# Optimization experiments

Measured on AMD Instinct MI355X. Metric: run time of the kernel, lower is better.

## Reference

```python
import jax, jax.numpy as jnp
import numpy as np

K = 3
TAU = 1.0
EPS = 1e-8


def _route_dense(z, k, tau):
    """RouterTopK forward -> dense combine weights [N, L].
    Matches torch: topk values, softmax(topv/tau). Softmax is permutation
    invariant so sorted top_k gives identical math to sorted=False."""
    topi = jax.lax.top_k(z, k)[1]                      # [N, k] int32
    topv = jnp.take_along_axis(z, topi, axis=1)        # [N, k]
    w = jax.nn.softmax(topv / (tau + EPS), axis=1)     # [N, k]
    N, L = z.shape
    dw = jnp.zeros((N, L), z.dtype)
    dw = dw.at[jnp.arange(N)[:, None], topi].add(w)
    return dw


def _apply_mixture(x, dw, W):
    """y[n] = sum_e dw[n,e] * (W[e] @ x[n]).  Loop over the small fixed
    expert count (12); equivalent math to the sort+grouped-GEMM dispatch."""
    y = jnp.zeros((x.shape[0], W.shape[1]), x.dtype)
    for e in range(W.shape[0]):
        y = y + (x @ W[e].T) * dw[:, e:e + 1]
    return y


def setup_inputs() -> dict:
    key = jax.random.key(0)
    ks = jax.random.split(key, 8)
    B, T, D_in, H, D_out, L, d_addr = 4, 2048, 1024, 4096, 1024, 12, 64

    def unitize(U):
        U = U - U.mean(axis=1, keepdims=True)
        return U / (jnp.linalg.norm(U, axis=1, keepdims=True) + EPS)

    x = jax.random.normal(ks[0], (B, T, D_in), jnp.float32)
    P_w = jax.random.normal(ks[1], (d_addr, D_in), jnp.float32) / np.sqrt(D_in)
    U1 = unitize(jax.random.normal(ks[2], (L, d_addr), jnp.float32))
    U2 = unitize(jax.random.normal(ks[3], (L, d_addr), jnp.float32))
    U3 = unitize(jax.random.normal(ks[4], (L, d_addr), jnp.float32))
    W1 = jax.random.normal(ks[5], (L, H, D_in), jnp.float32)
    W1 = W1 / jnp.linalg.norm(W1.reshape(L, -1), axis=1)[:, None, None]
    W2 = jax.random.normal(ks[6], (L, D_out, H), jnp.float32)
    W2 = W2 / jnp.linalg.norm(W2.reshape(L, -1), axis=1)[:, None, None]
    b2 = jax.random.normal(ks[7], (L, D_out), jnp.float32)
    b2 = b2 / jnp.linalg.norm(b2, axis=1, keepdims=True)
    return {"x": x, "P_w": P_w, "U1": U1, "U2": U2, "U3": U3,
            "W1": W1, "W2": W2, "b2": b2}


def reference(x, P_w, U1, U2, U3, W1, W2, b2):
    B, T, D = x.shape
    x_flat = x.reshape(B * T, D)                       # [N, D_in]
    x_addr = x_flat @ P_w.T                            # [N, d_addr]
    dw1 = _route_dense(x_addr @ U1.T, K, TAU)          # [N, L]
    dw2 = _route_dense(x_addr @ U2.T, K, TAU)
    dw3 = _route_dense(x_addr @ U3.T, K, TAU)
    h = _apply_mixture(x_flat, dw1, W1)                # [N, H]
    h = jax.nn.gelu(h, approximate=False)              # nn.GELU (exact)
    y = _apply_mixture(h, dw2, W2)                     # [N, D_out]
    y = y + dw3 @ b2                                   # grouped bias add
    return y.reshape(B, T, -1)
```

## Files before the change

kernel.cpp:

```cpp
#include <hip/hip_runtime.h>
#include <math.h>

#define DEVI __device__ __forceinline__
typedef unsigned short u16;
typedef unsigned int u32;
typedef unsigned char u8;
typedef float f32x4 __attribute__((ext_vector_type(4)));

static constexpr int CAP = 8192;

DEVI u16 f2b(float f) {
  u32 x = __builtin_bit_cast(u32, f);
  u32 r = (x + 0x7fffu + ((x >> 16) & 1u)) >> 16;
  return (u16)r;
}
DEVI float b2f(u16 u) { return __builtin_bit_cast(float, (u32)u << 16); }

DEVI u32 f2fp8(float f) {
  u32 x = __builtin_bit_cast(u32, f);
  u32 s = (x >> 24) & 0x80u;
  u32 ax = x & 0x7fffffffu;
  if (ax >= 0x43e80000u) return s | 0x7eu;
  if (ax < 0x3a800000u) return s;
  if (ax < 0x3c800000u) {
    float m = __builtin_bit_cast(float, ax) * 512.0f;
    return s | (u32)rintf(m);
  }
  u32 r = ax + 0x7ffffu + ((ax >> 20) & 1u);
  return s | (((r >> 23) - 120u) << 3) | ((r >> 20) & 7u);
}

DEVI void async16(const void* g, void* l) {
  __builtin_amdgcn_global_load_lds((const __attribute__((address_space(1))) void*)g,
                                   (__attribute__((address_space(3))) void*)l, 16, 0, 0);
}

__global__ void cvt8_k(const float* __restrict__ s0, u8* __restrict__ d0,
                       const float* __restrict__ s1, u8* __restrict__ d1, long n) {
  long nq0 = n / 4, nq = nq0 * 2;
  long stride = (long)gridDim.x * blockDim.x;
  for (long q = (long)blockIdx.x * blockDim.x + threadIdx.x; q < nq; q += stride) {
    long qi = q; const float* s = s0; u8* d = d0;
    if (qi >= nq0) { qi -= nq0; s = s1; d = d1; }
    float4 v = ((const float4*)s)[qi];
    uchar4 o;
    o.x = (u8)f2fp8(v.x * 1024.f); o.y = (u8)f2fp8(v.y * 1024.f);
    o.z = (u8)f2fp8(v.z * 1024.f); o.w = (u8)f2fp8(v.w * 1024.f);
    ((uchar4*)d)[qi] = o;
  }
}

__global__ __launch_bounds__(256) void xaddr2_k(
    const float* __restrict__ x, const float* __restrict__ Pw,
    double* __restrict__ xa_g, u8* __restrict__ xb) {
  __shared__ __align__(16) char sm[19584];
  float* xs  = (float*)sm;
  float* pws = (float*)(sm + 2176);

  const int tid = threadIdx.x;
  const int tok0 = blockIdx.x * 8;
  const int kbase = blockIdx.y * 512;
  const int tok = tid >> 5, dg = tid & 31;

  double a0 = 0, a1 = 0, a2 = 0, a3 = 0;

  const int rot0 = dg >> 3;
  const int rot1 = (dg >> 3) + 4;

  for (int kc = 0; kc < 8; ++kc) {
    const int k0 = kbase + kc * 64;
    if (tid < 128) {
      int t = tid >> 4, c4 = tid & 15;
      size_t goff = (size_t)(tok0 + t) * 1024 + k0 + c4 * 4;
      float4 v = *(const float4*)&x[goff];
      *(float4*)&xs[t * 68 + c4 * 4] = v;
      uchar4 o8;
      o8.x = (u8)f2fp8(v.x); o8.y = (u8)f2fp8(v.y);
      o8.z = (u8)f2fp8(v.z); o8.w = (u8)f2fp8(v.w);
      *(uchar4*)&xb[goff] = o8;
    }
#pragma unroll
    for (int j = 0; j < 4; ++j) {
      int f = tid + 256 * j;
      int pr = f >> 4, pc = f & 15;
      int pos = (pc + (pr >> 3)) & 15;
      *(float4*)&pws[pr * 68 + pos * 4] = *(const float4*)&Pw[(size_t)pr * 1024 + k0 + pc * 4];
    }
    __syncthreads();
    const float* xrow = &xs[tok * 68];
#pragma unroll
    for (int k4 = 0; k4 < 16; ++k4) {
      float4 xv = *(const float4*)&xrow[k4 * 4];
      float4 q0 = *(const float4*)&pws[dg * 68 + ((k4 + rot0) & 15) * 4];
      float4 q1 = *(const float4*)&pws[(dg + 32) * 68 + ((k4 + rot1) & 15) * 4];
      a0 += (double)xv.x * q0.x + (double)xv.y * q0.y;
      a1 += (double)xv.z * q0.z + (double)xv.w * q0.w;
      a2 += (double)xv.x * q1.x + (double)xv.y * q1.y;
      a3 += (double)xv.z * q1.z + (double)xv.w * q1.w;
    }
    __syncthreads();
  }

  size_t base = ((size_t)blockIdx.y * 8192 + (tok0 + tok)) * 64;
  xa_g[base + dg] = a0 + a1;
  xa_g[base + dg + 32] = a2 + a3;
}

__global__ __launch_bounds__(256) void route2_k(
    const double* __restrict__ xa_g,
    const float* __restrict__ U1, const float* __restrict__ U2, const float* __restrict__ U3,
    const float* __restrict__ b2,
    int* __restrict__ cnt, int* __restrict__ ltok, float* __restrict__ lwgt,
    float* __restrict__ out) {
  __shared__ double xa[16][66];
  __shared__ float us[36][68];
  __shared__ double zz[16][40];
  __shared__ int se[16][4];
  __shared__ float swg[16][4];

  const int tid = threadIdx.x;
  const int tok0 = blockIdx.x * 16;

  {
    const int tk = tid >> 4, j = tid & 15;
    const double* s0 = &xa_g[(size_t)(tok0 + tk) * 64 + j * 4];
    const double* s1 = s0 + (size_t)8192 * 64;
#pragma unroll
    for (int m = 0; m < 4; ++m) xa[tk][j * 4 + m] = s0[m] + s1[m];
  }
  if (tid < 144) {
#pragma unroll
    for (int j = 0; j < 4; ++j) {
      int f = tid * 4 + j;
      int r = f >> 4, c4 = f & 15;
      const float* U = (r < 12) ? (U1 + r * 64) : (r < 24 ? U2 + (r - 12) * 64 : U3 + (r - 24) * 64);
      *(float4*)&us[r][c4 * 4] = *(const float4*)&U[c4 * 4];
    }
  }
  __syncthreads();

#pragma unroll
  for (int rep = 0; rep < 3; ++rep) {
    int idx = tid + 256 * rep;
    if (idx < 576) {
      int tk = idx / 36, re = idx - tk * 36;
      double acc = 0;
      const double* xr = &xa[tk][0];
      const float* ur = &us[re][0];
      for (int k = 0; k < 64; ++k) acc += xr[k] * (double)ur[k];
      zz[tk][re] = acc;
    }
  }
  __syncthreads();

  if (tid < 48) {
    const int tk = tid & 15, r = tid >> 4;
    const double* z = &zz[tk][r * 12];
    double v0 = -1e300, v1 = -1e300, v2 = -1e300;
    int i0 = 0, i1 = 0, i2 = 0;
    for (int e = 0; e < 12; ++e) {
      double v = z[e];
      if (v > v0)      { v2 = v1; i2 = i1; v1 = v0; i1 = i0; v0 = v; i0 = e; }
      else if (v > v1) { v2 = v1; i2 = i1; v1 = v; i1 = e; }
      else if (v > v2) { v2 = v; i2 = e; }
    }
    const double inv_tau = 1.0 / (1.0 + 1e-8);
    double e1 = exp((v1 - v0) * inv_tau), e2 = exp((v2 - v0) * inv_tau);
    double s = 1.0 / (1.0 + e1 + e2);
    double w0 = s, w1 = e1 * s, w2 = e2 * s;
    int n = tok0 + tk;
    if (r < 2) {
      int jj3[3] = { i0, i1, i2 };
      double ww[3] = { w0, w1, w2 };
      for (int j = 0; j < 3; ++j) {
        int slot = (r * 3 + j) * 12 + jj3[j];
        int pos = atomicAdd(&cnt[slot], 1);
        ltok[slot * CAP + pos] = n;
        lwgt[slot * CAP + pos] = (float)ww[j];
      }
    } else {
      se[tk][0] = i0; se[tk][1] = i1; se[tk][2] = i2;
      swg[tk][0] = (float)w0; swg[tk][1] = (float)w1; swg[tk][2] = (float)w2;
    }
  }
  __syncthreads();

#pragma unroll
  for (int j = 0; j < 16; ++j) {
    int f = tid + 256 * j;
    int tk = f >> 8, c4 = f & 255;
    const float w0 = swg[tk][0], w1 = swg[tk][1], w2 = swg[tk][2];
    float4 a = *(const float4*)&b2[(size_t)se[tk][0] * 1024 + c4 * 4];
    float4 b = *(const float4*)&b2[(size_t)se[tk][1] * 1024 + c4 * 4];
    float4 d = *(const float4*)&b2[(size_t)se[tk][2] * 1024 + c4 * 4];
    float4 o;
    o.x = w0 * a.x + w1 * b.x + w2 * d.x;
    o.y = w0 * a.y + w1 * b.y + w2 * d.y;
    o.z = w0 * a.z + w1 * b.z + w2 * d.z;
    o.w = w0 * a.w + w1 * b.w + w2 * d.w;
    *(float4*)&out[(size_t)(tok0 + tk) * 1024 + c4 * 4] = o;
  }
}

__global__ void build_k(const int* __restrict__ cnt, int2* __restrict__ desc,
                        int* __restrict__ ntl) {
  int t = threadIdx.x;
  if (t < 6) {
    int nt = 0;
    for (int e = 0; e < 12; ++e) {
      int c = cnt[t * 12 + e];
      for (int s = 0; s < c; s += 128) { desc[t * 96 + nt] = make_int2(e, s); ++nt; }
    }
    ntl[t] = nt;
  }
}

template<int KB, int NOUT, bool ADD, typename CT>
__global__ __launch_bounds__(256, 5) void moe_gemm(
    const u8* __restrict__ A, const u8* __restrict__ W, CT* __restrict__ C,
    float outScale,
    const int* __restrict__ cnt12, const int* __restrict__ ltok12,
    const float* __restrict__ lwgt12,
    const int2* __restrict__ desc, const int* __restrict__ ntl) {
  unsigned lin = blockIdx.y * gridDim.x + blockIdx.x;
  unsigned q = (gridDim.x * gridDim.y) >> 3;
  unsigned swz = (lin & 7) * q + (lin >> 3);
  int tile = swz % gridDim.x;
  int ntile = swz / gridDim.x;
  if (tile >= *ntl) return;
  const int2 dd = desc[tile];
  const int e = dd.x, rowStart = dd.y;
  const int rows = min(128, cnt12[e] - rowStart);
  const int base = e * CAP + rowStart;

  __shared__ __align__(16) u8 As[2][8192];
  __shared__ __align__(16) u8 Bs[2][8192];

  const int tid = threadIdx.x;
  const int lane = tid & 63, w = tid >> 6;

  const int srcSwz = (((tid & 3) ^ ((tid >> 3) & 3)) * 16);
  const u8* aSrc[2]; const u8* bSrc[2];
  {
    int ra = tid >> 2;
    int t0 = ltok12[base + min(ra, rows - 1)];
    int t1 = ltok12[base + min(64 + ra, rows - 1)];
    aSrc[0] = A + (size_t)t0 * KB + srcSwz;
    aSrc[1] = A + (size_t)t1 * KB + srcSwz;
#pragma unroll
    for (int i = 0; i < 2; ++i) {
      int r = i * 64 + ra;
      bSrc[i] = W + ((size_t)e * NOUT + ntile * 128 + r) * KB + srcSwz;
    }
  }

  f32x4 acc[4][4] = {};
  const int wr = w >> 1, wc = w & 1;
  const int sxr = (lane >> 1) & 3;
  const int p8 = ((lane >> 4) & 1) * 8;
  const int roff0 = 16 * (((lane >> 5) | 0) ^ sxr) + p8;
  const int roff1 = 16 * (((lane >> 5) | 2) ^ sxr) + p8;
  constexpr int NT = KB / 64;

#define STAGE(kt_) do { int ko_ = (kt_) * 64; int b_ = (kt_) & 1;               \
    async16(aSrc[0] + ko_, &As[b_][tid * 16]);                                  \
    async16(aSrc[1] + ko_, &As[b_][(256 + tid) * 16]);                          \
    async16(bSrc[0] + ko_, &Bs[b_][tid * 16]);                                  \
    async16(bSrc[1] + ko_, &Bs[b_][(256 + tid) * 16]); } while (0)

  STAGE(0);
  __syncthreads();
  for (int kt = 0; kt < NT; ++kt) {
    if (kt + 1 < NT) STAGE(kt + 1);
    const u8* Ab = &As[kt & 1][0];
    const u8* Bb = &Bs[kt & 1][0];
#pragma unroll
    for (int kk = 0; kk < 2; ++kk) {
      const int ro = kk ? roff1 : roff0;
      long bf[4];
#pragma unroll
      for (int ni = 0; ni < 4; ++ni) {
        int rB = wc * 64 + ni * 16 + (lane & 15);
        bf[ni] = *(const long*)&Bb[rB * 64 + ro];
      }
#pragma unroll
      for (int mi = 0; mi < 4; ++mi) {
        int rA = wr * 64 + mi * 16 + (lane & 15);
        long af = *(const long*)&Ab[rA * 64 + ro];
#pragma unroll
        for (int ni = 0; ni < 4; ++ni)
          acc[mi][ni] = __builtin_amdgcn_mfma_f32_16x16x32_fp8_fp8(af, bf[ni], acc[mi][ni], 0, 0, 0);
      }
    }
    __syncthreads();
  }
#undef STAGE

#pragma unroll
  for (int mi = 0; mi < 4; ++mi) {
    int lr0 = wr * 64 + mi * 16 + ((lane >> 4) << 2);
#pragma unroll
    for (int rr = 0; rr < 4; ++rr) {
      int lrow = lr0 + rr;
      bool rowok = lrow < rows;
      int idx = base + (rowok ? lrow : 0);
      int tok = ltok12[idx];
      float wv = lwgt12[idx] * outScale;
      if constexpr (sizeof(CT) == 2) {
        u32* cp32 = (u32*)((u16*)C + (size_t)tok * NOUT + ntile * 128 + wc * 64 + (lane & 14));
#pragma unroll
        for (int ni = 0; ni < 4; ++ni) {
          float v = acc[mi][ni][rr] * wv;
          float vo = __shfl_xor(v, 1);
          if (rowok && !(lane & 1)) {
            float lo = v, hi = vo;
            if (ADD) {
              u32 curv = cp32[ni * 8];
              lo += b2f((u16)(curv & 0xffffu));
              hi += b2f((u16)(curv >> 16));
            }
            cp32[ni * 8] = (u32)f2b(lo) | ((u32)f2b(hi) << 16);
          }
        }
      } else {
        if (rowok) {
          float* cp = (float*)C + (size_t)tok * NOUT + ntile * 128 + wc * 64 + (lane & 15);
#pragma unroll
          for (int ni = 0; ni < 4; ++ni) {
            float val = acc[mi][ni][rr] * wv;
            float* p = cp + ni * 16;
            *p = ADD ? (*p + val) : val;
          }
        }
      }
    }
  }
}

DEVI float gelu1(float v) { return 0.5f * v * (1.0f + erff(v * 0.70710678118654752f)); }
__global__ void gelu8_k(const u32* __restrict__ h, uint2* __restrict__ h8, long n8) {
  long stride = (long)gridDim.x * blockDim.x;
  const uint4* hp = (const uint4*)h;
  for (long i = (long)blockIdx.x * blockDim.x + threadIdx.x; i < n8; i += stride) {
    uint4 v = hp[i];
    u32 words[4] = { v.x, v.y, v.z, v.w };
    u32 lo = 0, hi = 0;
#pragma unroll
    for (int j = 0; j < 4; ++j) {
      float f0 = b2f((u16)(words[j] & 0xffffu));
      float f1 = b2f((u16)(words[j] >> 16));
      u32 c0 = f2fp8(gelu1(f0) * 256.f);
      u32 c1 = f2fp8(gelu1(f1) * 256.f);
      u32 pair = c0 | (c1 << 8);
      if (j < 2) lo |= pair << (16 * j);
      else       hi |= pair << (16 * (j - 2));
    }
    h8[i] = make_uint2(lo, hi);
  }
}

extern "C" void kernel_launch(void* const* d_in, const int* in_sizes, int n_in,
                              void* d_out, int out_size, void* d_ws, size_t ws_size,
                              hipStream_t stream) {
  const float* x  = (const float*)d_in[0];
  const float* Pw = (const float*)d_in[1];
  const float* U1 = (const float*)d_in[2];
  const float* U2 = (const float*)d_in[3];
  const float* U3 = (const float*)d_in[4];
  const float* W1 = (const float*)d_in[5];
  const float* W2 = (const float*)d_in[6];
  const float* b2 = (const float*)d_in[7];
  float* out = (float*)d_out;

  char* ws = (char*)d_ws;
  size_t o = 0;
  u8*  W1b = (u8*)(ws + o); o += (size_t)12 * 4096 * 1024;
  u8*  W2b = (u8*)(ws + o); o += (size_t)12 * 1024 * 4096;
  u8*  xb  = (u8*)(ws + o); o += (size_t)8192 * 1024;
  u16* h   = (u16*)(ws + o); o += (size_t)8192 * 4096 * 2;
  u8*  h8  = (u8*)(ws + o); o += (size_t)8192 * 4096;
  double* xa_g = (double*)(ws + o); o += (size_t)2 * 8192 * 64 * 8;
  int* cnt = (int*)(ws + o); o += 512;
  int2* desc = (int2*)(ws + o); o += (size_t)6 * 96 * sizeof(int2);
  o = (o + 255) & ~(size_t)255;
  int* ntl = (int*)(ws + o); o += 256;
  int* ltok = (int*)(ws + o); o += (size_t)6 * 12 * CAP * 4;
  float* lwgt = (float*)(ws + o); o += (size_t)6 * 12 * CAP * 4;
  if (ws_size < o) return;

  hipMemsetAsync(cnt, 0, 512, stream);
  cvt8_k<<<4096, 256, 0, stream>>>(W1, W1b, W2, W2b, (long)12 * 4096 * 1024);
  xaddr2_k<<<dim3(1024, 2), 256, 0, stream>>>(x, Pw, xa_g, xb);
  route2_k<<<512, 256, 0, stream>>>(xa_g, U1, U2, U3, b2, cnt, ltok, lwgt, out);
  build_k<<<1, 64, 0, stream>>>(cnt, desc, ntl);

  const float s1 = 1.0f / 1024.f;
  const float s2 = 1.0f / (1024.f * 256.f);

  {
    dim3 g(80, 32);
    int s;
    s = 0; moe_gemm<1024, 4096, false, u16><<<g, 256, 0, stream>>>(xb, W1b, h, s1, cnt + s * 12, ltok + (size_t)s * 12 * CAP, lwgt + (size_t)s * 12 * CAP, desc + s * 96, ntl + s);
    s = 1; moe_gemm<1024, 4096, true , u16><<<g, 256, 0, stream>>>(xb, W1b, h, s1, cnt + s * 12, ltok + (size_t)s * 12 * CAP, lwgt + (size_t)s * 12 * CAP, desc + s * 96, ntl + s);
    s = 2; moe_gemm<1024, 4096, true , u16><<<g, 256, 0, stream>>>(xb, W1b, h, s1, cnt + s * 12, ltok + (size_t)s * 12 * CAP, lwgt + (size_t)s * 12 * CAP, desc + s * 96, ntl + s);
  }

  gelu8_k<<<2048, 256, 0, stream>>>((const u32*)h, (uint2*)h8, (long)8192 * 4096 / 8);

  {
    dim3 g(80, 8);
    int s;
    s = 3; moe_gemm<4096, 1024, true, float><<<g, 256, 0, stream>>>(h8, W2b, out, s2, cnt + s * 12, ltok + (size_t)s * 12 * CAP, lwgt + (size_t)s * 12 * CAP, desc + s * 96, ntl + s);
    s = 4; moe_gemm<4096, 1024, true, float><<<g, 256, 0, stream>>>(h8, W2b, out, s2, cnt + s * 12, ltok + (size_t)s * 12 * CAP, lwgt + (size_t)s * 12 * CAP, desc + s * 96, ntl + s);
    s = 5; moe_gemm<4096, 1024, true, float><<<g, 256, 0, stream>>>(h8, W2b, out, s2, cnt + s * 12, ltok + (size_t)s * 12 * CAP, lwgt + (size_t)s * 12 * CAP, desc + s * 96, ntl + s);
  }
}
```

Baseline: 1.019 ms.

## Pre-permute fp8 operands so GEMM loads 16-byte fragments; cache token routing in LDS

The fp8 conversion kernels for weights, x and the GELU output now write each 64-byte K chunk in an interleaved order. The MoE GEMM can then fetch both k-halves of an MFMA fragment with one 16-byte LDS read instead of two 8-byte reads, and all fragments are loaded before the MFMA chain. Per-tile token indices and weights are staged once in shared memory and reused in the address setup and epilogue, replacing repeated global reads. Launch bounds drop from 5 to 4 blocks per CU to allow more registers for the larger fragment set, at the cost of occupancy.

Result: faster. 910.7 us (-10.6%).

```diff
diff --git a/kernel.cpp b/kernel.cpp
--- a/kernel.cpp
+++ b/kernel.cpp
@@ -6,6 +6,7 @@
 typedef unsigned int u32;
 typedef unsigned char u8;
 typedef float f32x4 __attribute__((ext_vector_type(4)));
+typedef long lx2 __attribute__((ext_vector_type(2)));
 
 static constexpr int CAP = 8192;
 
@@ -35,18 +36,30 @@
                                    (__attribute__((address_space(3))) void*)l, 16, 0, 0);
 }
 
+DEVI u32 pack4(float a, float b, float c, float d, float sc) {
+  return f2fp8(a * sc) | (f2fp8(b * sc) << 8) | (f2fp8(c * sc) << 16) | (f2fp8(d * sc) << 24);
+}
+
 __global__ void cvt8_k(const float* __restrict__ s0, u8* __restrict__ d0,
                        const float* __restrict__ s1, u8* __restrict__ d1, long n) {
-  long nq0 = n / 4, nq = nq0 * 2;
+  long nc0 = n / 16, nc = nc0 * 2;
   long stride = (long)gridDim.x * blockDim.x;
-  for (long q = (long)blockIdx.x * blockDim.x + threadIdx.x; q < nq; q += stride) {
+  for (long q = (long)blockIdx.x * blockDim.x + threadIdx.x; q < nc; q += stride) {
     long qi = q; const float* s = s0; u8* d = d0;
-    if (qi >= nq0) { qi -= nq0; s = s1; d = d1; }
-    float4 v = ((const float4*)s)[qi];
-    uchar4 o;
-    o.x = (u8)f2fp8(v.x * 1024.f); o.y = (u8)f2fp8(v.y * 1024.f);
-    o.z = (u8)f2fp8(v.z * 1024.f); o.w = (u8)f2fp8(v.w * 1024.f);
-    ((uchar4*)d)[qi] = o;
+    if (qi >= nc0) { qi -= nc0; s = s1; d = d1; }
+    long b = qi >> 2; int c = (int)(qi & 3);
+    const float* p1 = s + b * 64 + c * 8;
+    const float* p2 = p1 + 32;
+    float4 v0 = *(const float4*)p1;
+    float4 v1 = *(const float4*)(p1 + 4);
+    float4 v2 = *(const float4*)p2;
+    float4 v3 = *(const float4*)(p2 + 4);
+    uint4 o;
+    o.x = pack4(v0.x, v0.y, v0.z, v0.w, 1024.f);
+    o.y = pack4(v1.x, v1.y, v1.z, v1.w, 1024.f);
+    o.z = pack4(v2.x, v2.y, v2.z, v2.w, 1024.f);
+    o.w = pack4(v3.x, v3.y, v3.z, v3.w, 1024.f);
+    *(uint4*)(d + b * 64 + c * 16) = o;
   }
 }
 
@@ -74,10 +87,10 @@
       size_t goff = (size_t)(tok0 + t) * 1024 + k0 + c4 * 4;
       float4 v = *(const float4*)&x[goff];
       *(float4*)&xs[t * 68 + c4 * 4] = v;
-      uchar4 o8;
-      o8.x = (u8)f2fp8(v.x); o8.y = (u8)f2fp8(v.y);
-      o8.z = (u8)f2fp8(v.z); o8.w = (u8)f2fp8(v.w);
-      *(uchar4*)&xb[goff] = o8;
+      int g = c4 >> 1;
+      int off = 16 * (g & 3) + 8 * (g >> 2) + 4 * (c4 & 1);
+      u32 o8 = pack4(v.x, v.y, v.z, v.w, 1.0f);
+      *(u32*)&xb[(size_t)(tok0 + t) * 1024 + k0 + off] = o8;
     }
 #pragma unroll
     for (int j = 0; j < 4; ++j) {
@@ -216,7 +229,7 @@
 }
 
 template<int KB, int NOUT, bool ADD, typename CT>
-__global__ __launch_bounds__(256, 5) void moe_gemm(
+__global__ __launch_bounds__(256, 4) void moe_gemm(
     const u8* __restrict__ A, const u8* __restrict__ W, CT* __restrict__ C,
     float outScale,
     const int* __restrict__ cnt12, const int* __restrict__ ltok12,
@@ -235,31 +248,30 @@
 
   __shared__ __align__(16) u8 As[2][8192];
   __shared__ __align__(16) u8 Bs[2][8192];
+  __shared__ int tokL[128];
+  __shared__ float wgtL[128];
 
   const int tid = threadIdx.x;
   const int lane = tid & 63, w = tid >> 6;
+  if (tid < 128) {
+    int li = min(tid, rows - 1);
+    tokL[tid] = ltok12[base + li];
+    wgtL[tid] = lwgt12[base + li];
+  }
+  __syncthreads();
 
   const int srcSwz = (((tid & 3) ^ ((tid >> 3) & 3)) * 16);
   const u8* aSrc[2]; const u8* bSrc[2];
-  {
-    int ra = tid >> 2;
-    int t0 = ltok12[base + min(ra, rows - 1)];
-    int t1 = ltok12[base + min(64 + ra, rows - 1)];
-    aSrc[0] = A + (size_t)t0 * KB + srcSwz;
-    aSrc[1] = A + (size_t)t1 * KB + srcSwz;
-#pragma unroll
-    for (int i = 0; i < 2; ++i) {
-      int r = i * 64 + ra;
-      bSrc[i] = W + ((size_t)e * NOUT + ntile * 128 + r) * KB + srcSwz;
-    }
+#pragma unroll
+  for (int i = 0; i < 2; ++i) {
+    int r = i * 64 + (tid >> 2);
+    aSrc[i] = A + (size_t)tokL[min(r, rows - 1)] * KB + srcSwz;
+    bSrc[i] = W + ((size_t)e * NOUT + ntile * 128 + r) * KB + srcSwz;
   }
 
   f32x4 acc[4][4] = {};
   const int wr = w >> 1, wc = w & 1;
-  const int sxr = (lane >> 1) & 3;
-  const int p8 = ((lane >> 4) & 1) * 8;
-  const int roff0 = 16 * (((lane >> 5) | 0) ^ sxr) + p8;
-  const int roff1 = 16 * (((lane >> 5) | 2) ^ sxr) + p8;
+  const int roff = 16 * ((((lane >> 4) & 3)) ^ ((lane >> 1) & 3));
   constexpr int NT = KB / 64;
 
 #define STAGE(kt_) do { int ko_ = (kt_) * 64; int b_ = (kt_) & 1;               \
@@ -274,24 +286,27 @@
     if (kt + 1 < NT) STAGE(kt + 1);
     const u8* Ab = &As[kt & 1][0];
     const u8* Bb = &Bs[kt & 1][0];
-#pragma unroll
-    for (int kk = 0; kk < 2; ++kk) {
-      const int ro = kk ? roff1 : roff0;
-      long bf[4];
-#pragma unroll
-      for (int ni = 0; ni < 4; ++ni) {
-        int rB = wc * 64 + ni * 16 + (lane & 15);
-        bf[ni] = *(const long*)&Bb[rB * 64 + ro];
-      }
-#pragma unroll
-      for (int mi = 0; mi < 4; ++mi) {
-        int rA = wr * 64 + mi * 16 + (lane & 15);
-        long af = *(const long*)&Ab[rA * 64 + ro];
-#pragma unroll
-        for (int ni = 0; ni < 4; ++ni)
-          acc[mi][ni] = __builtin_amdgcn_mfma_f32_16x16x32_fp8_fp8(af, bf[ni], acc[mi][ni], 0, 0, 0);
-      }
-    }
+    lx2 bv[4], av[4];
+#pragma unroll
+    for (int ni = 0; ni < 4; ++ni) {
+      int rB = wc * 64 + ni * 16 + (lane & 15);
+      bv[ni] = *(const lx2*)&Bb[rB * 64 + roff];
+    }
+#pragma unroll
+    for (int mi = 0; mi < 4; ++mi) {
+      int rA = wr * 64 + mi * 16 + (lane & 15);
+      av[mi] = *(const lx2*)&Ab[rA * 64 + roff];
+    }
+#pragma unroll
+    for (int mi = 0; mi < 4; ++mi)
+#pragma unroll
+      for (int ni = 0; ni < 4; ++ni)
+        acc[mi][ni] = __builtin_amdgcn_mfma_f32_16x16x32_fp8_fp8(av[mi].x, bv[ni].x, acc[mi][ni], 0, 0, 0);
+#pragma unroll
+    for (int mi = 0; mi < 4; ++mi)
+#pragma unroll
+      for (int ni = 0; ni < 4; ++ni)
+        acc[mi][ni] = __builtin_amdgcn_mfma_f32_16x16x32_fp8_fp8(av[mi].y, bv[ni].y, acc[mi][ni], 0, 0, 0);
     __syncthreads();
   }
 #undef STAGE
@@ -303,9 +318,8 @@
     for (int rr = 0; rr < 4; ++rr) {
       int lrow = lr0 + rr;
       bool rowok = lrow < rows;
-      int idx = base + (rowok ? lrow : 0);
-      int tok = ltok12[idx];
-      float wv = lwgt12[idx] * outScale;
+      int tok = tokL[lrow];
+      float wv = wgtL[lrow] * outScale;
       if constexpr (sizeof(CT) == 2) {
         u32* cp32 = (u32*)((u16*)C + (size_t)tok * NOUT + ntile * 128 + wc * 64 + (lane & 14));
 #pragma unroll
@@ -338,7 +352,7 @@
 }
 
 DEVI float gelu1(float v) { return 0.5f * v * (1.0f + erff(v * 0.70710678118654752f)); }
-__global__ void gelu8_k(const u32* __restrict__ h, uint2* __restrict__ h8, long n8) {
+__global__ void gelu8_k(const u32* __restrict__ h, u8* __restrict__ h8, long n8) {
   long stride = (long)gridDim.x * blockDim.x;
   const uint4* hp = (const uint4*)h;
   for (long i = (long)blockIdx.x * blockDim.x + threadIdx.x; i < n8; i += stride) {
@@ -355,7 +369,9 @@
       if (j < 2) lo |= pair << (16 * j);
       else       hi |= pair << (16 * (j - 2));
     }
-    h8[i] = make_uint2(lo, hi);
+    long b = i >> 3; int g = (int)(i & 7);
+    u32* dst = (u32*)(h8 + b * 64 + 16 * (g & 3) + 8 * (g >> 2));
+    dst[0] = lo; dst[1] = hi;
   }
 }
 
@@ -405,7 +421,7 @@
     s = 2; moe_gemm<1024, 4096, true , u16><<<g, 256, 0, stream>>>(xb, W1b, h, s1, cnt + s * 12, ltok + (size_t)s * 12 * CAP, lwgt + (size_t)s * 12 * CAP, desc + s * 96, ntl + s);
   }
 
-  gelu8_k<<<2048, 256, 0, stream>>>((const u32*)h, (uint2*)h8, (long)8192 * 4096 / 8);
+  gelu8_k<<<2048, 256, 0, stream>>>((const u32*)h, h8, (long)8192 * 4096 / 8);
 
   {
     dim3 g(80, 8);
```
